# Kernel optimization log

Hardware: AMD Instinct MI355X
Metric: run time of the kernel (lower is better)

## Reference

```python
import jax, jax.numpy as jnp
import numpy as np

MARGIN = 1.0


def setup_inputs() -> dict:
    key = jax.random.key(0)
    k1, k2 = jax.random.split(key)
    N, D, C = 8192, 128, 64
    embeddings = jax.random.normal(k1, (N, D), dtype=jnp.float32)
    labels = jax.random.randint(k2, (N,), 0, C, dtype=jnp.int64)
    return {"embeddings": embeddings, "labels": labels}


def _pairwise_euclidean(x):
    # ||xi - xj|| via Gram trick; safe sqrt (zero grad at 0, matches masked use)
    sq = jnp.sum(x * x, axis=1)                      # [N]
    d2 = sq[:, None] + sq[None, :] - 2.0 * (x @ x.T)  # [N, N]
    d2 = jnp.maximum(d2, 0.0)
    pos = d2 > 0.0
    return jnp.where(pos, jnp.sqrt(jnp.where(pos, d2, 1.0)), 0.0)


def reference(embeddings, labels):
    N = embeddings.shape[0]
    dist = _pairwise_euclidean(embeddings)            # [N, N]
    same = labels[:, None] == labels[None, :]         # [N, N]
    eye = jnp.eye(N, dtype=bool)
    pos_mask = same & ~eye
    neg_mask = ~same

    neg_inf = jnp.float32(-jnp.inf)
    pos_inf = jnp.float32(jnp.inf)
    hardest_pos = jnp.max(jnp.where(pos_mask, dist, neg_inf), axis=1)  # [N]
    hardest_neg = jnp.min(jnp.where(neg_mask, dist, pos_inf), axis=1)  # [N]

    has_pos = jnp.any(pos_mask, axis=1)
    has_neg = jnp.any(neg_mask, axis=1)
    tl = jax.nn.relu(hardest_pos - hardest_neg + MARGIN)               # [N]
    valid = has_pos & has_neg & (tl > 0.0)

    total = jnp.sum(jnp.where(valid, tl, 0.0))
    count = jnp.sum(valid)
    return jnp.where(count > 0, total / jnp.maximum(count, 1).astype(total.dtype), jnp.float32(0.0))
```

## Files before the change

kernel.cpp:

```cpp
#include <hip/hip_runtime.h>
#include <hip/hip_bf16.h>
#include <math.h>

#define NN 8192
#define DD 128
#define BM 256
#define BN 64
#define NPART 16
#define JRANGE (NN / NPART)
#define NTILES (JRANGE / BN)

typedef __attribute__((ext_vector_type(8))) short bf16x8;
typedef __attribute__((ext_vector_type(4))) float f32x4;

#define WS_SJC 0
#define WS_HPK 65536
#define WS_HNK (WS_HPK + NN * 4)
#define WS_AB  (WS_HNK + NN * 4)

__device__ __forceinline__ unsigned fkey(float f) {
    unsigned u = __float_as_uint(f);
    return (u & 0x80000000u) ? ~u : (u | 0x80000000u);
}
__device__ __forceinline__ float fkey_inv(unsigned k) {
    unsigned u = (k & 0x80000000u) ? (k ^ 0x80000000u) : ~k;
    return __uint_as_float(u);
}
__device__ __forceinline__ ushort f2bf(float x) {
    __hip_bfloat16 h = __float2bfloat16(x);
    return *reinterpret_cast<ushort*>(&h);
}

__global__ __launch_bounds__(256)
void prepq_k(const float* __restrict__ emb, const int* __restrict__ lab,
             float2* __restrict__ sjc, unsigned* __restrict__ hpK,
             unsigned* __restrict__ hnK, ushort* __restrict__ aB) {
    const int lane = threadIdx.x & 63;
    const int w    = threadIdx.x >> 6;
    const int half = lane >> 5;
    const int l32  = lane & 31;
    const int row  = blockIdx.x * 8 + w * 2 + half;

    float4 v = reinterpret_cast<const float4*>(emb)[row * 32 + l32];
    float s = 0.f;
    s = fmaf(v.x, v.x, s); s = fmaf(v.y, v.y, s);
    s = fmaf(v.z, v.z, s); s = fmaf(v.w, v.w, s);
#pragma unroll
    for (int off = 1; off < 32; off <<= 1) s += __shfl_xor(s, off, 64);

    ushort4 b;
    b.x = f2bf(v.x); b.y = f2bf(v.y); b.z = f2bf(v.z); b.w = f2bf(v.w);
    const int idx = (row >> 4) * 2048 + (l32 >> 3) * 512 + ((l32 >> 1) & 3) * 128
                  + (row & 15) * 8 + (l32 & 1) * 4;
    *reinterpret_cast<ushort4*>(aB + idx) = b;

    if (l32 == 0) sjc[row] = make_float2(s, __int_as_float(lab[row]));
    if (threadIdx.x < 8) {
        int r0 = blockIdx.x * 8 + threadIdx.x;
        hpK[r0] = 0x007FFFFFu;
        hnK[r0] = 0xFF800000u;
    }
}

__global__ __launch_bounds__(256, 2)
void hardest_k(const ushort* __restrict__ aB, const float2* __restrict__ sjc,
               unsigned* __restrict__ hpK, unsigned* __restrict__ hnK) {
    const int tid  = threadIdx.x;
    const int w    = tid >> 6;
    const int lane = tid & 63;
    const int lrow = lane & 15;
    const int lk   = lane >> 4;
    const int ib   = (int)blockIdx.x >> 4;
    const int part = (int)blockIdx.x & 15;
    const int i0   = ib * BM;
    const int jbeg = part * JRANGE;

    bf16x8 a[4][4];
#pragma unroll
    for (int s = 0; s < 4; ++s) {
        const int gA = ib * 16 + w * 4 + s;
#pragma unroll
        for (int q = 0; q < 4; ++q)
            a[s][q] = *reinterpret_cast<const bf16x8*>(&aB[gA * 2048 + q * 512 + lane * 8]);
    }
    int   li[4][4];
    float hpg[4][4], hng[4][4];
#pragma unroll
    for (int s = 0; s < 4; ++s)
#pragma unroll
        for (int t = 0; t < 4; ++t) {
            float2 md = sjc[i0 + w * 64 + s * 16 + lk * 4 + t];
            li[s][t]  = __float_as_int(md.y);
            hpg[s][t] = -INFINITY;
            hng[s][t] =  INFINITY;
        }

#pragma unroll 1
    for (int jt = 0; jt < NTILES; ++jt) {
        const int j0 = jbeg + jt * BN;
#pragma unroll
        for (int c = 0; c < 4; ++c) {
            const int gB = (j0 >> 4) + c;
            const ushort* bp = &aB[gB * 2048 + lane * 8];
            bf16x8 b0 = *reinterpret_cast<const bf16x8*>(bp);
            bf16x8 b1 = *reinterpret_cast<const bf16x8*>(bp + 512);
            bf16x8 b2 = *reinterpret_cast<const bf16x8*>(bp + 1024);
            bf16x8 b3 = *reinterpret_cast<const bf16x8*>(bp + 1536);
            float2 sv = sjc[j0 + c * 16 + lrow];
            f32x4 acc[4];
            f32x4 zero = {0.f, 0.f, 0.f, 0.f};
#pragma unroll
            for (int s = 0; s < 4; ++s) acc[s] = zero;
#pragma unroll
            for (int s = 0; s < 4; ++s) {
                acc[s] = __builtin_amdgcn_mfma_f32_16x16x32_bf16(a[s][0], b0, acc[s], 0, 0, 0);
                acc[s] = __builtin_amdgcn_mfma_f32_16x16x32_bf16(a[s][1], b1, acc[s], 0, 0, 0);
                acc[s] = __builtin_amdgcn_mfma_f32_16x16x32_bf16(a[s][2], b2, acc[s], 0, 0, 0);
                acc[s] = __builtin_amdgcn_mfma_f32_16x16x32_bf16(a[s][3], b3, acc[s], 0, 0, 0);
            }
            const float sqj = sv.x;
            const int   lj  = __float_as_int(sv.y);
#pragma unroll
            for (int s = 0; s < 4; ++s)
#pragma unroll
                for (int t = 0; t < 4; ++t) {
                    float gg = fmaf(-2.f, acc[s][t], sqj);
                    bool same = (li[s][t] == lj);
                    hpg[s][t] = fmaxf(hpg[s][t], same ? gg : -INFINITY);
                    hng[s][t] = fminf(hng[s][t], same ? INFINITY : gg);
                }
        }
    }

#pragma unroll
    for (int off = 1; off < 16; off <<= 1)
#pragma unroll
        for (int s = 0; s < 4; ++s)
#pragma unroll
            for (int t = 0; t < 4; ++t) {
                hpg[s][t] = fmaxf(hpg[s][t], __shfl_xor(hpg[s][t], off, 64));
                hng[s][t] = fminf(hng[s][t], __shfl_xor(hng[s][t], off, 64));
            }
    if (lrow == 0) {
#pragma unroll
        for (int s = 0; s < 4; ++s)
#pragma unroll
            for (int t = 0; t < 4; ++t) {
                int i = i0 + w * 64 + s * 16 + lk * 4 + t;
                atomicMax(&hpK[i], fkey(hpg[s][t]));
                atomicMin(&hnK[i], fkey(hng[s][t]));
            }
    }
}

__global__ __launch_bounds__(1024)
void final_k(const unsigned* __restrict__ hpK, const unsigned* __restrict__ hnK,
             const float2* __restrict__ sjc, float* __restrict__ out) {
    float total = 0.f, cnt = 0.f;
    for (int i = threadIdx.x; i < NN; i += 1024) {
        float hp = fkey_inv(hpK[i]);
        float hn = fkey_inv(hnK[i]);
        float s  = sjc[i].x;
        float hp2 = s + hp, hn2 = s + hn;
        float hpd = (hp2 == -INFINITY) ? -INFINITY : sqrtf(fmaxf(hp2, 0.f));
        float hnd = (hn2 ==  INFINITY) ?  INFINITY : sqrtf(fmaxf(hn2, 0.f));
        float tl = hpd - hnd + 1.0f;
        if (tl > 0.f) { total += tl; cnt += 1.f; }
    }
#pragma unroll
    for (int off = 1; off < 64; off <<= 1) {
        total += __shfl_xor(total, off, 64);
        cnt   += __shfl_xor(cnt,   off, 64);
    }
    __shared__ float sT[16], sC[16];
    int wave = threadIdx.x >> 6;
    if ((threadIdx.x & 63) == 0) { sT[wave] = total; sC[wave] = cnt; }
    __syncthreads();
    if (threadIdx.x == 0) {
        float T = 0.f, Cn = 0.f;
#pragma unroll
        for (int k = 0; k < 16; ++k) { T += sT[k]; Cn += sC[k]; }
        out[0] = (Cn > 0.f) ? T / Cn : 0.f;
    }
}

extern "C" void kernel_launch(void* const* d_in, const int* in_sizes, int n_in,
                              void* d_out, int out_size, void* d_ws, size_t ws_size,
                              hipStream_t stream) {
    const float* emb = (const float*)d_in[0];
    const int*   lab = (const int*)d_in[1];
    char* ws = (char*)d_ws;
    float2*   sjc = (float2*)(ws + WS_SJC);
    unsigned* hpK = (unsigned*)(ws + WS_HPK);
    unsigned* hnK = (unsigned*)(ws + WS_HNK);
    ushort*   aB  = (ushort*)(ws + WS_AB);

    prepq_k<<<dim3(NN / 8), dim3(256), 0, stream>>>(emb, lab, sjc, hpK, hnK, aB);
    hardest_k<<<dim3((NN / BM) * NPART), dim3(256), 0, stream>>>(aB, sjc, hpK, hnK);
    final_k<<<dim3(1), dim3(1024), 0, stream>>>(hpK, hnK, sjc, (float*)d_out);
}
```

Baseline: 41.18 us.

## Exploit distance-matrix symmetry by computing only upper-triangular tile blocks

Replaces the full row-block by column-partition grid with a triangular schedule over 256x256 super-blocks. Each off-diagonal tile updates both the row-side and column-side hardest positive/negative via atomics, and diagonal tiles skip sub-blocks below the diagonal. This roughly halves the MFMA work, at the cost of per-column cross-lane reductions and many more atomics per tile. The squared norm is now folded in on both sides, so the final kernel no longer needs it.

Result: slower. 60.29 us (+46.4%).

```diff
diff --git a/kernel.cpp b/kernel.cpp
--- a/kernel.cpp
+++ b/kernel.cpp
@@ -4,11 +4,9 @@
 
 #define NN 8192
 #define DD 128
-#define BM 256
-#define BN 64
-#define NPART 16
-#define JRANGE (NN / NPART)
-#define NTILES (JRANGE / BN)
+#define NSB 32
+#define NOFF (NSB * (NSB - 1) / 2)
+#define NBLK (NOFF + NSB / 2)
 
 typedef __attribute__((ext_vector_type(8))) short bf16x8;
 typedef __attribute__((ext_vector_type(4))) float f32x4;
@@ -62,73 +60,91 @@
     }
 }
 
-__global__ __launch_bounds__(256, 2)
-void hardest_k(const ushort* __restrict__ aB, const float2* __restrict__ sjc,
-               unsigned* __restrict__ hpK, unsigned* __restrict__ hnK) {
-    const int tid  = threadIdx.x;
-    const int w    = tid >> 6;
-    const int lane = tid & 63;
-    const int lrow = lane & 15;
-    const int lk   = lane >> 4;
-    const int ib   = (int)blockIdx.x >> 4;
-    const int part = (int)blockIdx.x & 15;
-    const int i0   = ib * BM;
-    const int jbeg = part * JRANGE;
+template<bool DIAG>
+__device__ __forceinline__ void do_tile(int bi, int bj, int w, int lane,
+                                        int lrow, int lk,
+                                        const ushort* __restrict__ aB,
+                                        const float2* __restrict__ sjc,
+                                        unsigned* __restrict__ hpK,
+                                        unsigned* __restrict__ hnK) {
+    const int i0  = bi * 256;
+    const int j0b = bj * 256;
 
     bf16x8 a[4][4];
 #pragma unroll
     for (int s = 0; s < 4; ++s) {
-        const int gA = ib * 16 + w * 4 + s;
+        const int gA = bi * 16 + w * 4 + s;
 #pragma unroll
         for (int q = 0; q < 4; ++q)
             a[s][q] = *reinterpret_cast<const bf16x8*>(&aB[gA * 2048 + q * 512 + lane * 8]);
     }
     int   li[4][4];
-    float hpg[4][4], hng[4][4];
+    float sqA[4][4], hpg[4][4], hng[4][4];
 #pragma unroll
     for (int s = 0; s < 4; ++s)
 #pragma unroll
         for (int t = 0; t < 4; ++t) {
             float2 md = sjc[i0 + w * 64 + s * 16 + lk * 4 + t];
+            sqA[s][t] = md.x;
             li[s][t]  = __float_as_int(md.y);
             hpg[s][t] = -INFINITY;
             hng[s][t] =  INFINITY;
         }
 
 #pragma unroll 1
-    for (int jt = 0; jt < NTILES; ++jt) {
-        const int j0 = jbeg + jt * BN;
-#pragma unroll
-        for (int c = 0; c < 4; ++c) {
-            const int gB = (j0 >> 4) + c;
-            const ushort* bp = &aB[gB * 2048 + lane * 8];
-            bf16x8 b0 = *reinterpret_cast<const bf16x8*>(bp);
-            bf16x8 b1 = *reinterpret_cast<const bf16x8*>(bp + 512);
-            bf16x8 b2 = *reinterpret_cast<const bf16x8*>(bp + 1024);
-            bf16x8 b3 = *reinterpret_cast<const bf16x8*>(bp + 1536);
-            float2 sv = sjc[j0 + c * 16 + lrow];
-            f32x4 acc[4];
-            f32x4 zero = {0.f, 0.f, 0.f, 0.f};
-#pragma unroll
-            for (int s = 0; s < 4; ++s) acc[s] = zero;
-#pragma unroll
-            for (int s = 0; s < 4; ++s) {
+    for (int c = 0; c < 16; ++c) {
+        const int gB = bj * 16 + c;
+        const ushort* bp = &aB[gB * 2048 + lane * 8];
+        bf16x8 b0 = *reinterpret_cast<const bf16x8*>(bp);
+        bf16x8 b1 = *reinterpret_cast<const bf16x8*>(bp + 512);
+        bf16x8 b2 = *reinterpret_cast<const bf16x8*>(bp + 1024);
+        bf16x8 b3 = *reinterpret_cast<const bf16x8*>(bp + 1536);
+        float2 sv = sjc[j0b + c * 16 + lrow];
+        const float sqj = sv.x;
+        const int   lj  = __float_as_int(sv.y);
+
+        f32x4 acc[4];
+        f32x4 zero = {0.f, 0.f, 0.f, 0.f};
+#pragma unroll
+        for (int s = 0; s < 4; ++s) acc[s] = zero;
+#pragma unroll
+        for (int s = 0; s < 4; ++s) {
+            if (!DIAG || (w * 4 + s) <= c) {
                 acc[s] = __builtin_amdgcn_mfma_f32_16x16x32_bf16(a[s][0], b0, acc[s], 0, 0, 0);
                 acc[s] = __builtin_amdgcn_mfma_f32_16x16x32_bf16(a[s][1], b1, acc[s], 0, 0, 0);
                 acc[s] = __builtin_amdgcn_mfma_f32_16x16x32_bf16(a[s][2], b2, acc[s], 0, 0, 0);
                 acc[s] = __builtin_amdgcn_mfma_f32_16x16x32_bf16(a[s][3], b3, acc[s], 0, 0, 0);
             }
-            const float sqj = sv.x;
-            const int   lj  = __float_as_int(sv.y);
-#pragma unroll
-            for (int s = 0; s < 4; ++s)
+        }
+        float cp[4], cn[4];
+#pragma unroll
+        for (int s = 0; s < 4; ++s) { cp[s] = -INFINITY; cn[s] = INFINITY; }
+#pragma unroll
+        for (int s = 0; s < 4; ++s) {
+            if (!DIAG || (w * 4 + s) <= c) {
 #pragma unroll
                 for (int t = 0; t < 4; ++t) {
-                    float gg = fmaf(-2.f, acc[s][t], sqj);
+                    float d2 = fmaf(-2.f, acc[s][t], sqA[s][t] + sqj);
                     bool same = (li[s][t] == lj);
-                    hpg[s][t] = fmaxf(hpg[s][t], same ? gg : -INFINITY);
-                    hng[s][t] = fminf(hng[s][t], same ? INFINITY : gg);
+                    float vp = same ? d2 : -INFINITY;
+                    float vn = same ? INFINITY : d2;
+                    hpg[s][t] = fmaxf(hpg[s][t], vp);
+                    hng[s][t] = fminf(hng[s][t], vn);
+                    cp[s] = fmaxf(cp[s], vp);
+                    cn[s] = fminf(cn[s], vn);
                 }
+            }
+        }
+        float cpv = fmaxf(fmaxf(cp[0], cp[1]), fmaxf(cp[2], cp[3]));
+        float cnv = fminf(fminf(cn[0], cn[1]), fminf(cn[2], cn[3]));
+        cpv = fmaxf(cpv, __shfl_xor(cpv, 16, 64));
+        cpv = fmaxf(cpv, __shfl_xor(cpv, 32, 64));
+        cnv = fminf(cnv, __shfl_xor(cnv, 16, 64));
+        cnv = fminf(cnv, __shfl_xor(cnv, 32, 64));
+        if ((!DIAG || w * 4 <= c) && lk == 0) {
+            int j = j0b + c * 16 + lrow;
+            atomicMax(&hpK[j], fkey(cpv));
+            atomicMin(&hnK[j], fkey(cnv));
         }
     }
 
@@ -153,15 +169,33 @@
     }
 }
 
+__global__ __launch_bounds__(256, 2)
+void hardest_k(const ushort* __restrict__ aB, const float2* __restrict__ sjc,
+               unsigned* __restrict__ hpK, unsigned* __restrict__ hnK) {
+    const int w    = threadIdx.x >> 6;
+    const int lane = threadIdx.x & 63;
+    const int lrow = lane & 15;
+    const int lk   = lane >> 4;
+
+    if ((int)blockIdx.x < NOFF) {
+        int rem = (int)blockIdx.x, bi = 0;
+        while (rem >= NSB - 1 - bi) { rem -= NSB - 1 - bi; ++bi; }
+        const int bj = bi + 1 + rem;
+        do_tile<false>(bi, bj, w, lane, lrow, lk, aB, sjc, hpK, hnK);
+    } else {
+        const int p = (int)blockIdx.x - NOFF;
+        do_tile<true>(2 * p,     2 * p,     w, lane, lrow, lk, aB, sjc, hpK, hnK);
+        do_tile<true>(2 * p + 1, 2 * p + 1, w, lane, lrow, lk, aB, sjc, hpK, hnK);
+    }
+}
+
 __global__ __launch_bounds__(1024)
 void final_k(const unsigned* __restrict__ hpK, const unsigned* __restrict__ hnK,
-             const float2* __restrict__ sjc, float* __restrict__ out) {
+             float* __restrict__ out) {
     float total = 0.f, cnt = 0.f;
     for (int i = threadIdx.x; i < NN; i += 1024) {
-        float hp = fkey_inv(hpK[i]);
-        float hn = fkey_inv(hnK[i]);
-        float s  = sjc[i].x;
-        float hp2 = s + hp, hn2 = s + hn;
+        float hp2 = fkey_inv(hpK[i]);
+        float hn2 = fkey_inv(hnK[i]);
         float hpd = (hp2 == -INFINITY) ? -INFINITY : sqrtf(fmaxf(hp2, 0.f));
         float hnd = (hn2 ==  INFINITY) ?  INFINITY : sqrtf(fmaxf(hn2, 0.f));
         float tl = hpd - hnd + 1.0f;
@@ -196,6 +230,6 @@
     ushort*   aB  = (ushort*)(ws + WS_AB);
 
     prepq_k<<<dim3(NN / 8), dim3(256), 0, stream>>>(emb, lab, sjc, hpK, hnK, aB);
-    hardest_k<<<dim3((NN / BM) * NPART), dim3(256), 0, stream>>>(aB, sjc, hpK, hnK);
-    final_k<<<dim3(1), dim3(1024), 0, stream>>>(hpK, hnK, sjc, (float*)d_out);
-}
+    hardest_k<<<dim3(NBLK), dim3(256), 0, stream>>>(aB, sjc, hpK, hnK);
+    final_k<<<dim3(1), dim3(1024), 0, stream>>>(hpK, hnK, (float*)d_out);
+}
```
